# Performance work log

Hardware: AMD Instinct MI355X
Metric: run time of the kernel (lower is better)

Reference implementation:

```python
import jax, jax.numpy as jnp
import numpy as np

N_NODES = 100000
N_EDGES = 1200000
N_DIM = 64


def setup_inputs() -> dict:
    key = jax.random.key(0)
    k1, k2, k3 = jax.random.split(key, 3)
    all_emb = jax.random.normal(k1, (N_NODES, N_DIM), dtype=jnp.float32) * 0.1
    edge_vals = jax.random.uniform(k2, (N_EDGES,), dtype=jnp.float32)
    edge_index = jax.random.randint(k3, (2, N_EDGES), 0, N_NODES, dtype=jnp.int64)
    return {"all_emb": all_emb, "edge_vals": edge_vals, "edge_index": edge_index, "n_layers": 3}


def _spmm(edge_vals, edge_index, x):
    # sparse.mm: out[dst] += val * x[src]; edge_index[0]=row(dst), edge_index[1]=col(src)
    dst, src = edge_index[0], edge_index[1]
    msgs = edge_vals[:, None] * x[src]          # [E, D] gather + scale
    return jax.ops.segment_sum(msgs, dst, num_segments=x.shape[0])


def reference(all_emb, edge_vals, edge_index, n_layers):
    # Fused layer-mean accumulation (avoids stacking all intermediates).
    emb = all_emb
    acc = all_emb
    for _ in range(n_layers):
        emb = _spmm(edge_vals, edge_index, emb)
        acc = acc + emb
    return acc / jnp.float32(n_layers + 1)
```

## Files before the change

### kernel.cpp

```cpp
#include <hip/hip_runtime.h>
#include <hip/hip_bf16.h>
#include <hip/hip_fp16.h>

#define D 64
#define P2_GRID 512
#define KITER 10
#define CHUNK (KITER*256)
#define KMAX 512
#define CAP 4096
#define SCAP 4608
#define CASTB 392

__device__ __forceinline__ unsigned f32_to_bf16_rne(float f) {
    unsigned u = __float_as_uint(f);
    return (u + 0x7FFFu + ((u >> 16) & 1u)) >> 16;
}
__device__ __forceinline__ float bfu(unsigned short w) {
    return __uint_as_float((unsigned)w << 16);
}
__device__ __forceinline__ float hv(unsigned s) {
    return __half2float(__ushort_as_half((unsigned short)(s >> 17)));
}

__global__ __launch_bounds__(256) void p2_bin_cast(const int* __restrict__ ei,
                                                   const float* __restrict__ vals,
                                                   int* __restrict__ gcur,
                                                   unsigned long long* __restrict__ region,
                                                   const float4* __restrict__ emb4,
                                                   uint2* __restrict__ x0,
                                                   int n4, int E, int K) {
    __shared__ unsigned long long stage[CHUNK];
    __shared__ int hist[KMAX], sstart[KMAX], sbase[KMAX];
    __shared__ int wsum[4], woff[4];

    if (blockIdx.x >= P2_GRID) {
        int i0 = (blockIdx.x - P2_GRID) * 256 + threadIdx.x;
        for (int i = i0; i < n4; i += CASTB * 256) {
            float4 v = emb4[i];
            uint2 o;
            o.x = f32_to_bf16_rne(v.x) | (f32_to_bf16_rne(v.y) << 16);
            o.y = f32_to_bf16_rne(v.z) | (f32_to_bf16_rne(v.w) << 16);
            x0[i] = o;
        }
        return;
    }

    int t  = threadIdx.x;
    int c0 = blockIdx.x * CHUNK;
    int cnt = E - c0; if (cnt > CHUNK) cnt = CHUNK; if (cnt < 0) cnt = 0;

    hist[t] = 0; hist[t + 256] = 0;
    __syncthreads();

    unsigned long long ent[KITER];
    int rk[KITER];
    #pragma unroll
    for (int k = 0; k < KITER; ++k) {
        int i = t + k * 256;
        rk[k] = -1;
        if (i < cnt) {
            int e   = c0 + i;
            int dst = ei[e];
            int src = ei[E + e];
            unsigned h16 = (unsigned)__half_as_ushort(__float2half(vals[e]));
            int b = dst >> 8;
            ent[k] = ((unsigned long long)b << 41)
                   | ((unsigned long long)h16 << 25)
                   | ((unsigned long long)(dst & 0xFF) << 17)
                   | (unsigned long long)src;
            rk[k] = atomicAdd(&hist[b], 1);
        }
    }
    __syncthreads();

    int h0 = hist[2 * t], h1 = hist[2 * t + 1];
    int p  = h0 + h1;
    int lane = t & 63, w = t >> 6;
    int x = p;
    #pragma unroll
    for (int off = 1; off < 64; off <<= 1) {
        int y = __shfl_up(x, off, 64);
        if (lane >= off) x += y;
    }
    if (lane == 63) wsum[w] = x;
    __syncthreads();
    if (t < 4) {
        int e = 0;
        for (int i = 0; i < t; ++i) e += wsum[i];
        woff[t] = e;
    }
    __syncthreads();
    int excl = x - p + woff[w];
    sstart[2 * t]     = excl;
    sstart[2 * t + 1] = excl + h0;
    __syncthreads();

    for (int b = t; b < K; b += 256)
        sbase[b] = hist[b] ? atomicAdd(&gcur[b], hist[b]) : 0;

    #pragma unroll
    for (int k = 0; k < KITER; ++k) {
        if (rk[k] >= 0)
            stage[sstart[(int)(ent[k] >> 41)] + rk[k]] = ent[k];
    }
    __syncthreads();

    for (int i = t; i < cnt; i += 256) {
        unsigned long long e = stage[i];
        int b = (int)(e >> 41);
        int gidx = sbase[b] + (i - sstart[b]);
        if (gidx < CAP)
            region[((size_t)b << 12) | gidx] = e;
    }
}

__global__ __launch_bounds__(1024) void p3_csr(const unsigned long long* __restrict__ region,
                                               const int* __restrict__ gcur,
                                               unsigned* __restrict__ gslots,
                                               unsigned* __restrict__ rowinfo,
                                               int N) {
    __shared__ unsigned outstage[SCAP];
    __shared__ int rcnt[256], rstart[256];
    __shared__ int wsum[4], woff[4];
    __shared__ int stot;
    int b = blockIdx.x, t = threadIdx.x;
    int cnt = gcur[b]; if (cnt > CAP) cnt = CAP;
    const unsigned long long* reg = region + ((size_t)b << 12);

    if (t < 256) rcnt[t] = 0;
    __syncthreads();

    unsigned long long ent[4];
    int rk[4];
    #pragma unroll
    for (int k = 0; k < 4; ++k) {
        int i = t + k * 1024;
        rk[k] = -1;
        if (i < cnt) {
            ent[k] = reg[i];
            rk[k]  = atomicAdd(&rcnt[(int)(ent[k] >> 17) & 0xFF], 1);
        }
    }
    __syncthreads();

    int rc = 0, rcp = 0, x = 0, rs = 0;
    int lane = t & 63, w = t >> 6;
    if (t < 256) {
        rc  = rcnt[t]; if (rc > 56) rc = 56;
        rcp = (rc + 7) & ~7;
        x = rcp;
        #pragma unroll
        for (int off = 1; off < 64; off <<= 1) {
            int y = __shfl_up(x, off, 64);
            if (lane >= off) x += y;
        }
        if (lane == 63) wsum[w] = x;
    }
    __syncthreads();
    if (t < 4) {
        int e = 0;
        for (int i = 0; i < t; ++i) e += wsum[i];
        woff[t] = e;
    }
    __syncthreads();
    if (t < 256) {
        rs = x - rcp + woff[w];
        rstart[t] = rs;
        if (t == 255) stot = rs + rcp;
    }
    __syncthreads();

    #pragma unroll
    for (int k = 0; k < 4; ++k) {
        if (rk[k] >= 0 && rk[k] < 56) {
            int pos = rstart[(int)(ent[k] >> 17) & 0xFF] + rk[k];
            if (pos < SCAP)
                outstage[pos] = ((unsigned)((ent[k] >> 25) & 0x7FFF) << 17)
                              | (unsigned)(ent[k] & 0x1FFFF);
        }
    }
    if (t < 256) {
        for (int i = rs + rc; i < rs + rcp; ++i)
            if (i >= 0 && i < SCAP) outstage[i] = 0u;
    }
    __syncthreads();

    int ptot = stot; if (ptot > SCAP) ptot = SCAP;
    size_t gb = (size_t)b * SCAP;
    for (int i = t; i < ptot; i += 1024)
        gslots[gb + i] = outstage[i];
    if (t < 256) {
        int row = (b << 8) | t;
        if (row < N) {
            int ni = rcp >> 3;
            if (rs >= SCAP) ni = 0;
            else if (rs + (ni << 3) > SCAP) ni = (SCAP - rs) >> 3;
            rowinfo[row] = ((unsigned)(gb + (size_t)rs) << 4) | (unsigned)ni;
        }
    }
}

__global__ __launch_bounds__(256) void spmm8(const unsigned short* __restrict__ xs,
                                             const unsigned* __restrict__ gslots,
                                             const unsigned* __restrict__ rowinfo,
                                             unsigned short* __restrict__ nexts,
                                             const unsigned short* __restrict__ x0s,
                                             const unsigned short* __restrict__ h1s,
                                             float* __restrict__ outf,
                                             int mode, int N) {
    int gid = blockIdx.x * blockDim.x + threadIdx.x;
    int row = __builtin_amdgcn_readfirstlane(gid >> 6);
    if (row >= N) return;
    int lane = gid & 63;
    unsigned info = rowinfo[row];
    int niter = (int)(info & 15u);
    const unsigned* s = gslots + (info >> 4);

    float sum0 = 0.f, sum1 = 0.f;
    if (niter > 0) {
        unsigned a[8];
        unsigned short u[8];
        #pragma unroll
        for (int j = 0; j < 8; ++j) a[j] = s[j];
        #pragma unroll
        for (int j = 0; j < 8; ++j)
            u[j] = xs[((size_t)(a[j] & 0x1FFFFu) << 6) | lane];
        for (int it = 1; it < niter; ++it) {
            s += 8;
            unsigned b[8];
            unsigned short v[8];
            #pragma unroll
            for (int j = 0; j < 8; ++j) b[j] = s[j];
            #pragma unroll
            for (int j = 0; j < 8; ++j)
                v[j] = xs[((size_t)(b[j] & 0x1FFFFu) << 6) | lane];
            #pragma unroll
            for (int j = 0; j < 8; ++j) {
                float m = hv(a[j]) * bfu(u[j]);
                if (j & 1) sum1 += m; else sum0 += m;
            }
            #pragma unroll
            for (int j = 0; j < 8; ++j) { a[j] = b[j]; u[j] = v[j]; }
        }
        #pragma unroll
        for (int j = 0; j < 8; ++j) {
            float m = hv(a[j]) * bfu(u[j]);
            if (j & 1) sum1 += m; else sum0 += m;
        }
    }
    float sum = sum0 + sum1;

    int o = (row << 6) | lane;
    if (mode != 2) {
        nexts[o] = (unsigned short)f32_to_bf16_rne(sum);
    } else {
        outf[o] = (bfu(x0s[o]) + bfu(h1s[o]) + bfu(xs[o]) + sum) * 0.25f;
    }
}

extern "C" void kernel_launch(void* const* d_in, const int* in_sizes, int n_in,
                              void* d_out, int out_size, void* d_ws, size_t ws_size,
                              hipStream_t stream) {
    const float* all_emb   = (const float*)d_in[0];
    const float* edge_vals = (const float*)d_in[1];
    const int*   edge_idx  = (const int*)d_in[2];

    const int E = in_sizes[1];
    const int n = out_size;
    const int N = n / D;
    const int K = (N + 255) >> 8;
    float* out = (float*)d_out;

    unsigned long long* region = (unsigned long long*)d_ws;
    unsigned* gslots  = (unsigned*)(region + (size_t)K * CAP);
    unsigned* rowinfo = gslots + (size_t)K * SCAP;
    int*      gcur    = (int*)(rowinfo + N);
    unsigned* X0      = (unsigned*)(gcur + ((K + 1) & ~1));
    unsigned* X1      = X0 + n / 2;
    unsigned* X2      = X1 + n / 2;

    const int TB = 256;
    const int grid_spmm = (N * 64 + TB - 1) / TB;

    hipMemsetAsync(gcur, 0, (size_t)K * sizeof(int), stream);
    p2_bin_cast<<<P2_GRID + CASTB, TB, 0, stream>>>(edge_idx, edge_vals, gcur, region,
                                                    (const float4*)all_emb, (uint2*)X0,
                                                    n / 4, E, K);
    p3_csr<<<K, 1024, 0, stream>>>(region, gcur, gslots, rowinfo, N);

    spmm8<<<grid_spmm, TB, 0, stream>>>((const unsigned short*)X0, gslots, rowinfo,
                                        (unsigned short*)X1, nullptr, nullptr, nullptr, 0, N);
    spmm8<<<grid_spmm, TB, 0, stream>>>((const unsigned short*)X1, gslots, rowinfo,
                                        (unsigned short*)X2, nullptr, nullptr, nullptr, 1, N);
    spmm8<<<grid_spmm, TB, 0, stream>>>((const unsigned short*)X2, gslots, rowinfo,
                                        nullptr, (const unsigned short*)X0,
                                        (const unsigned short*)X1, out, 2, N);
}
```

Baseline: 228.9 us.

## Split wave into four edge groups gathering 4 bf16 columns per lane

The SpMM kernel now has each 64-lane wave split into four 16-lane groups. Each group handles different edges of the same row, and each lane gathers 4 bf16 values (8 bytes) instead of one 2-byte value. The partial sums are combined with cross-lane xor shuffles, and the first 16 lanes write vectorized results. This is meant to cut the number of narrow gather instructions and make each memory access wider. In exchange it drops the explicit software prefetch pipelining and adds shuffle reductions, with only a quarter of the lanes active on the final store.

```diff
diff --git a/kernel.cpp b/kernel.cpp
--- a/kernel.cpp
+++ b/kernel.cpp
@@ -15,8 +15,11 @@
     unsigned u = __float_as_uint(f);
     return (u + 0x7FFFu + ((u >> 16) & 1u)) >> 16;
 }
-__device__ __forceinline__ float bfu(unsigned short w) {
-    return __uint_as_float((unsigned)w << 16);
+__device__ __forceinline__ float bflo(unsigned u) {
+    return __uint_as_float(u << 16);
+}
+__device__ __forceinline__ float bfhi(unsigned u) {
+    return __uint_as_float(u & 0xFFFF0000u);
 }
 __device__ __forceinline__ float hv(unsigned s) {
     return __half2float(__ushort_as_half((unsigned short)(s >> 17)));
@@ -200,61 +203,60 @@
     }
 }
 
-__global__ __launch_bounds__(256) void spmm8(const unsigned short* __restrict__ xs,
-                                             const unsigned* __restrict__ gslots,
-                                             const unsigned* __restrict__ rowinfo,
-                                             unsigned short* __restrict__ nexts,
-                                             const unsigned short* __restrict__ x0s,
-                                             const unsigned short* __restrict__ h1s,
-                                             float* __restrict__ outf,
-                                             int mode, int N) {
+__global__ __launch_bounds__(256) void spmm4e(const uint2* __restrict__ xs2,
+                                              const unsigned* __restrict__ gslots,
+                                              const unsigned* __restrict__ rowinfo,
+                                              uint2* __restrict__ nexts2,
+                                              const uint2* __restrict__ x0s2,
+                                              const uint2* __restrict__ h1s2,
+                                              float4* __restrict__ outf4,
+                                              int mode, int N) {
     int gid = blockIdx.x * blockDim.x + threadIdx.x;
     int row = __builtin_amdgcn_readfirstlane(gid >> 6);
     if (row >= N) return;
     int lane = gid & 63;
+    int q = lane >> 4;
+    int p = lane & 15;
     unsigned info = rowinfo[row];
     int niter = (int)(info & 15u);
     const unsigned* s = gslots + (info >> 4);
 
-    float sum0 = 0.f, sum1 = 0.f;
-    if (niter > 0) {
-        unsigned a[8];
-        unsigned short u[8];
-        #pragma unroll
-        for (int j = 0; j < 8; ++j) a[j] = s[j];
-        #pragma unroll
-        for (int j = 0; j < 8; ++j)
-            u[j] = xs[((size_t)(a[j] & 0x1FFFFu) << 6) | lane];
-        for (int it = 1; it < niter; ++it) {
-            s += 8;
-            unsigned b[8];
-            unsigned short v[8];
-            #pragma unroll
-            for (int j = 0; j < 8; ++j) b[j] = s[j];
-            #pragma unroll
-            for (int j = 0; j < 8; ++j)
-                v[j] = xs[((size_t)(b[j] & 0x1FFFFu) << 6) | lane];
-            #pragma unroll
-            for (int j = 0; j < 8; ++j) {
-                float m = hv(a[j]) * bfu(u[j]);
-                if (j & 1) sum1 += m; else sum0 += m;
-            }
-            #pragma unroll
-            for (int j = 0; j < 8; ++j) { a[j] = b[j]; u[j] = v[j]; }
-        }
-        #pragma unroll
-        for (int j = 0; j < 8; ++j) {
-            float m = hv(a[j]) * bfu(u[j]);
-            if (j & 1) sum1 += m; else sum0 += m;
-        }
-    }
-    float sum = sum0 + sum1;
-
-    int o = (row << 6) | lane;
-    if (mode != 2) {
-        nexts[o] = (unsigned short)f32_to_bf16_rne(sum);
-    } else {
-        outf[o] = (bfu(x0s[o]) + bfu(h1s[o]) + bfu(xs[o]) + sum) * 0.25f;
+    float a0 = 0.f, a1 = 0.f, a2 = 0.f, a3 = 0.f;
+    for (int it = 0; it < niter; ++it, s += 8) {
+        unsigned s0 = s[0], s1 = s[1], s2 = s[2], s3 = s[3],
+                 s4 = s[4], s5 = s[5], s6 = s[6], s7 = s[7];
+        unsigned wa = (q & 2) ? ((q & 1) ? s3 : s2) : ((q & 1) ? s1 : s0);
+        unsigned wb = (q & 2) ? ((q & 1) ? s7 : s6) : ((q & 1) ? s5 : s4);
+        uint2 ga = xs2[((size_t)(wa & 0x1FFFFu) << 4) | p];
+        uint2 gb = xs2[((size_t)(wb & 0x1FFFFu) << 4) | p];
+        float va = hv(wa), vb = hv(wb);
+        a0 += va * bflo(ga.x); a1 += va * bfhi(ga.x);
+        a2 += va * bflo(ga.y); a3 += va * bfhi(ga.y);
+        a0 += vb * bflo(gb.x); a1 += vb * bfhi(gb.x);
+        a2 += vb * bflo(gb.y); a3 += vb * bfhi(gb.y);
+    }
+
+    a0 += __shfl_xor(a0, 16, 64); a1 += __shfl_xor(a1, 16, 64);
+    a2 += __shfl_xor(a2, 16, 64); a3 += __shfl_xor(a3, 16, 64);
+    a0 += __shfl_xor(a0, 32, 64); a1 += __shfl_xor(a1, 32, 64);
+    a2 += __shfl_xor(a2, 32, 64); a3 += __shfl_xor(a3, 32, 64);
+
+    if (lane < 16) {
+        int o = (row << 4) | p;
+        if (mode != 2) {
+            uint2 r;
+            r.x = f32_to_bf16_rne(a0) | (f32_to_bf16_rne(a1) << 16);
+            r.y = f32_to_bf16_rne(a2) | (f32_to_bf16_rne(a3) << 16);
+            nexts2[o] = r;
+        } else {
+            uint2 x0 = x0s2[o], h1 = h1s2[o], x2 = xs2[o];
+            float4 r;
+            r.x = (bflo(x0.x) + bflo(h1.x) + bflo(x2.x) + a0) * 0.25f;
+            r.y = (bfhi(x0.x) + bfhi(h1.x) + bfhi(x2.x) + a1) * 0.25f;
+            r.z = (bflo(x0.y) + bflo(h1.y) + bflo(x2.y) + a2) * 0.25f;
+            r.w = (bfhi(x0.y) + bfhi(h1.y) + bfhi(x2.y) + a3) * 0.25f;
+            outf4[o] = r;
+        }
     }
 }
 
@@ -288,11 +290,11 @@
                                                     n / 4, E, K);
     p3_csr<<<K, 1024, 0, stream>>>(region, gcur, gslots, rowinfo, N);
 
-    spmm8<<<grid_spmm, TB, 0, stream>>>((const unsigned short*)X0, gslots, rowinfo,
-                                        (unsigned short*)X1, nullptr, nullptr, nullptr, 0, N);
-    spmm8<<<grid_spmm, TB, 0, stream>>>((const unsigned short*)X1, gslots, rowinfo,
-                                        (unsigned short*)X2, nullptr, nullptr, nullptr, 1, N);
-    spmm8<<<grid_spmm, TB, 0, stream>>>((const unsigned short*)X2, gslots, rowinfo,
-                                        nullptr, (const unsigned short*)X0,
-                                        (const unsigned short*)X1, out, 2, N);
-}
+    spmm4e<<<grid_spmm, TB, 0, stream>>>((const uint2*)X0, gslots, rowinfo,
+                                         (uint2*)X1, nullptr, nullptr, nullptr, 0, N);
+    spmm4e<<<grid_spmm, TB, 0, stream>>>((const uint2*)X1, gslots, rowinfo,
+                                         (uint2*)X2, nullptr, nullptr, nullptr, 1, N);
+    spmm4e<<<grid_spmm, TB, 0, stream>>>((const uint2*)X2, gslots, rowinfo,
+                                         nullptr, (const uint2*)X0,
+                                         (const uint2*)X1, (float4*)out, 2, N);
+}
```

After: 233.5 us. 1.02x slower.
